# Kernel optimization log

Hardware: AMD Instinct MI355X
Metric: run time of the kernel (lower is better)

## Reference

```python
import jax, jax.numpy as jnp
import numpy as np

B, LQ, C = 4, 4096, 384
NH, NL, NP = 6, 1, 4
HL, WL = 64, 64
LV = HL * WL
DH = C // NH
EPS = 1e-6


def layer_norm(x, g, b):
    mu = jnp.mean(x, axis=-1, keepdims=True)
    var = jnp.mean(jnp.square(x - mu), axis=-1, keepdims=True)
    return (x - mu) * jax.lax.rsqrt(var + EPS) * g + b


def ms_deform_attn_core(value, spatial_shapes, level_start_index, loc, attn_w):
    # value [B,LV,NH,DH]; loc [B,LQ,NH,NL,NP,2] in [0,1]; attn_w [B,LQ,NH,NL,NP]
    ss = np.asarray(spatial_shapes)
    lsi = np.asarray(level_start_index)
    Bv, _, nH, dh = value.shape
    Lq = loc.shape[1]
    nP = loc.shape[4]
    out = jnp.zeros((Bv, Lq, nH, dh), value.dtype)
    for l in range(loc.shape[3]):
        Hl, Wl = int(ss[l, 0]), int(ss[l, 1])
        st = int(lsi[l])
        vflat = value[:, st:st + Hl * Wl]  # [B, Hl*Wl, nH, dh]
        xy = loc[:, :, :, l]               # [B,LQ,nH,NP,2]
        # grid_sample(align_corners=False): pixel = loc * size - 0.5
        x = xy[..., 0] * Wl - 0.5
        y = xy[..., 1] * Hl - 0.5
        x0 = jnp.floor(x)
        y0 = jnp.floor(y)
        wx = x - x0
        wy = y - y0
        x0i = x0.astype(jnp.int32)
        y0i = y0.astype(jnp.int32)

        def gather(xi, yi):
            # zero padding outside the feature map (padding_mode='zeros')
            valid = (xi >= 0) & (xi < Wl) & (yi >= 0) & (yi < Hl)
            idx = jnp.clip(yi, 0, Hl - 1) * Wl + jnp.clip(xi, 0, Wl - 1)  # [B,LQ,nH,NP]
            idx2 = idx.transpose(0, 1, 3, 2).reshape(Bv, Lq * nP, nH)
            g = jnp.take_along_axis(vflat, idx2[..., None], axis=1)       # [B,LQ*NP,nH,dh]
            g = g.reshape(Bv, Lq, nP, nH, dh).transpose(0, 1, 3, 2, 4)    # [B,LQ,nH,NP,dh]
            return g * valid[..., None].astype(value.dtype)

        samp = (gather(x0i, y0i) * ((1 - wx) * (1 - wy))[..., None]
                + gather(x0i + 1, y0i) * (wx * (1 - wy))[..., None]
                + gather(x0i, y0i + 1) * ((1 - wx) * wy)[..., None]
                + gather(x0i + 1, y0i + 1) * (wx * wy)[..., None])
        out = out + jnp.einsum('bqhpd,bqhp->bqhd', samp, attn_w[:, :, :, l])
    return out.reshape(Bv, Lq, nH * dh)


def setup_inputs() -> dict:
    key = jax.random.key(0)
    ks = jax.random.split(key, 12)
    s = 0.02
    return {
        'query': jax.random.normal(ks[0], (B, LQ, C), jnp.float32),
        'reference_points': jax.random.uniform(ks[1], (B, LQ, NL, 2), dtype=jnp.float32),
        'feat': jax.random.normal(ks[2], (B, LV, C), jnp.float32),
        'spatial_shapes': jnp.array([[HL, WL]], jnp.int32),
        'level_start_index': jnp.array([0], jnp.int32),
        'ln_q_g': jnp.ones((C,), jnp.float32), 'ln_q_b': jnp.zeros((C,), jnp.float32),
        'ln_f_g': jnp.ones((C,), jnp.float32), 'ln_f_b': jnp.zeros((C,), jnp.float32),
        'gamma': jax.random.normal(ks[3], (C,), jnp.float32) * 0.1,
        'Wv': jax.random.normal(ks[4], (C, C), jnp.float32) * s,
        'bv': jnp.zeros((C,), jnp.float32),
        'Wo': jax.random.normal(ks[5], (C, NH * NL * NP * 2), jnp.float32) * s,
        'bo': jax.random.normal(ks[6], (NH * NL * NP * 2,), jnp.float32) * 0.5,
        'Wa': jax.random.normal(ks[7], (C, NH * NL * NP), jnp.float32) * s,
        'ba': jnp.zeros((NH * NL * NP,), jnp.float32),
        'Wout': jax.random.normal(ks[8], (C, C), jnp.float32) * s,
        'bout': jnp.zeros((C,), jnp.float32),
    }


def reference(query, reference_points, feat, spatial_shapes, level_start_index,
              ln_q_g, ln_q_b, ln_f_g, ln_f_b, gamma,
              Wv, bv, Wo, bo, Wa, ba, Wout, bout):
    q = layer_norm(query, ln_q_g, ln_q_b)
    f = layer_norm(feat, ln_f_g, ln_f_b)
    value = (f @ Wv + bv).reshape(B, LV, NH, DH)
    offsets = (q @ Wo + bo).reshape(B, LQ, NH, NL, NP, 2)
    attn_w = jax.nn.softmax((q @ Wa + ba).reshape(B, LQ, NH, NL * NP), axis=-1)
    attn_w = attn_w.reshape(B, LQ, NH, NL, NP)
    # offset normalizer is (W, H) per level
    norm = jnp.stack([spatial_shapes[:, 1], spatial_shapes[:, 0]], -1).astype(jnp.float32)
    loc = reference_points[:, :, None, :, None, :] + offsets / norm[None, None, None, :, None, :]
    attn = ms_deform_attn_core(value, spatial_shapes, level_start_index, loc, attn_w)
    attn = attn @ Wout + bout
    return query + gamma * attn
```

## Files before the change

kernel.cpp:

```cpp
#include <hip/hip_runtime.h>
#include <math.h>

#define B_    4
#define LQ_   4096
#define C_    384
#define NH_   6
#define NP_   4
#define HL_   64
#define WL_   64
#define LV_   (HL_ * WL_)
#define ROWS_ (B_ * LQ_)
#define EPS_  1e-6f
#define NOFF_ 48
#define NLOG_ 24

typedef unsigned short u16;
typedef __bf16 bf16x8 __attribute__((ext_vector_type(8)));
typedef float  f32x4  __attribute__((ext_vector_type(4)));

__device__ __forceinline__ float bf2f(u16 v) {
    unsigned int u = ((unsigned int)v) << 16;
    return __uint_as_float(u);
}
__device__ __forceinline__ u16 f2bf(float f) {
    unsigned int u = __float_as_uint(f);
    u += 0x7fff + ((u >> 16) & 1);
    return (u16)(u >> 16);
}

__device__ __forceinline__ f32x4 mfma16(bf16x8 a, bf16x8 b, f32x4 c) {
    return __builtin_amdgcn_mfma_f32_16x16x32_bf16(a, b, c, 0, 0, 0);
}

__device__ __forceinline__ void gl_lds16(const u16* g, u16* l) {
    __builtin_amdgcn_global_load_lds(
        (const __attribute__((address_space(1))) unsigned int*)g,
        (__attribute__((address_space(3))) unsigned int*)l, 16, 0, 0);
}

#define LN_BLOCKS_   8192
#define PREP_BLOCKS_ 1273

__global__ __launch_bounds__(256) void ln_prep(
    const float* __restrict__ query, const float* __restrict__ feat,
    const float* __restrict__ qg, const float* __restrict__ qbv,
    const float* __restrict__ fg, const float* __restrict__ fbv,
    u16* __restrict__ qout, u16* __restrict__ fout,
    const float* __restrict__ Wv, const float* __restrict__ Wout,
    const float* __restrict__ Wo, const float* __restrict__ Wa,
    const float* __restrict__ bo, const float* __restrict__ ba,
    u16* __restrict__ WvT, u16* __restrict__ WoutT, u16* __restrict__ WcT,
    float* __restrict__ bias_c)
{
    if (blockIdx.x < LN_BLOCKS_) {
        int wid  = threadIdx.x >> 6;
        int lane = threadIdx.x & 63;
        int row  = blockIdx.x * 4 + wid;
        const float *src, *g, *bsh;
        u16* dst;
        int r;
        if (row < ROWS_) { src = query; g = qg; bsh = qbv; dst = qout; r = row; }
        else             { src = feat;  g = fg; bsh = fbv; dst = fout; r = row - ROWS_; }

        const float* x = src + (size_t)r * C_;
        float v[6];
        float s = 0.f;
#pragma unroll
        for (int k = 0; k < 6; ++k) { v[k] = x[lane + 64 * k]; s += v[k]; }
#pragma unroll
        for (int off = 32; off; off >>= 1) s += __shfl_xor(s, off);
        float mu = s * (1.f / C_);

        float s2 = 0.f;
#pragma unroll
        for (int k = 0; k < 6; ++k) { float d = v[k] - mu; s2 += d * d; }
#pragma unroll
        for (int off = 32; off; off >>= 1) s2 += __shfl_xor(s2, off);
        float rs = rsqrtf(s2 * (1.f / C_) + EPS_);

        u16* y = dst + (size_t)r * C_;
#pragma unroll
        for (int k = 0; k < 6; ++k) {
            int c = lane + 64 * k;
            y[c] = f2bf((v[k] - mu) * rs * g[c] + bsh[c]);
        }
    } else {
        const int KN = 384 * 384;
        int idx = (blockIdx.x - LN_BLOCKS_) * 256 + threadIdx.x;
        if (idx < KN) {
            int n = idx / 384, k = idx - n * 384;
            WvT[idx] = f2bf(Wv[k * 384 + n]);
        } else if (idx < 2 * KN) {
            int t = idx - KN;
            int n = t / 384, k = t - n * 384;
            WoutT[t] = f2bf(Wout[k * 384 + n]);
        } else if (idx < 2 * KN + 80 * 384) {
            int t = idx - 2 * KN;
            int n = t / 384, k = t - n * 384;
            float v = (n < 48) ? Wo[k * 48 + n] : (n < 72 ? Wa[k * 24 + (n - 48)] : 0.f);
            WcT[t] = f2bf(v);
        } else if (idx < 2 * KN + 80 * 384 + 80) {
            int n = idx - (2 * KN + 80 * 384);
            bias_c[n] = (n < 48) ? bo[n] : (n < 72 ? ba[n - 48] : 0.f);
        }
    }
}

__global__ __launch_bounds__(256) void gemm_combined(
    const u16* __restrict__ fb, const u16* __restrict__ qb,
    const u16* __restrict__ WvT, const u16* __restrict__ WcT,
    const float* __restrict__ bv, const float* __restrict__ bias_c,
    u16* __restrict__ valb, float* __restrict__ offs, float* __restrict__ logits)
{
    const int K = 384;
    __shared__ __align__(16) u16 As[128 * 32];
    __shared__ __align__(16) u16 Bs[128 * 32];

    int g    = blockIdx.x;
    int tid  = threadIdx.x;
    int lane = tid & 63, wid = tid >> 6;
    int fr = lane & 15, quad = lane >> 4;

    int srow = tid >> 2;
    int scol = (tid & 3) * 8;

    if (g < 384) {
        int m0 = (g / 3) * 128, n0 = (g % 3) * 128;
        const u16* agp0 = fb  + (size_t)(m0 + srow) * K + scol;
        const u16* agp1 = fb  + (size_t)(m0 + 64 + srow) * K + scol;
        const u16* bgp0 = WvT + (size_t)(n0 + srow) * K + scol;
        const u16* bgp1 = WvT + (size_t)(n0 + 64 + srow) * K + scol;
        u16* al0 = As + tid * 8;  u16* al1 = As + 2048 + tid * 8;
        u16* bl0 = Bs + tid * 8;  u16* bl1 = Bs + 2048 + tid * 8;

        int wm = (wid >> 1) * 64, wn = (wid & 1) * 64;

        f32x4 zero = {0.f, 0.f, 0.f, 0.f};
        f32x4 acc[4][4];
#pragma unroll
        for (int i = 0; i < 4; ++i)
#pragma unroll
            for (int j = 0; j < 4; ++j) acc[i][j] = zero;

        for (int k0 = 0; k0 < K; k0 += 32) {
            gl_lds16(agp0 + k0, al0);
            gl_lds16(agp1 + k0, al1);
            gl_lds16(bgp0 + k0, bl0);
            gl_lds16(bgp1 + k0, bl1);
            __syncthreads();
            bf16x8 af[4], bfr[4];
#pragma unroll
            for (int i = 0; i < 4; ++i)
                af[i] = *(bf16x8*)&As[(wm + i * 16 + fr) * 32 + quad * 8];
#pragma unroll
            for (int j = 0; j < 4; ++j)
                bfr[j] = *(bf16x8*)&Bs[(wn + j * 16 + fr) * 32 + quad * 8];
#pragma unroll
            for (int i = 0; i < 4; ++i)
#pragma unroll
                for (int j = 0; j < 4; ++j)
                    acc[i][j] = mfma16(af[i], bfr[j], acc[i][j]);
            __syncthreads();
        }

#pragma unroll
        for (int i = 0; i < 4; ++i) {
            int row = m0 + wm + i * 16 + quad * 4;
#pragma unroll
            for (int j = 0; j < 4; ++j) {
                int col = n0 + wn + j * 16 + fr;
                float bcol = bv[col];
#pragma unroll
                for (int r = 0; r < 4; ++r)
                    valb[(size_t)(row + r) * C_ + col] = f2bf(acc[i][j][r] + bcol);
            }
        }
    } else {
        int m0 = (g - 384) * 128;
        const u16* agp0 = qb + (size_t)(m0 + srow) * K + scol;
        const u16* agp1 = qb + (size_t)(m0 + 64 + srow) * K + scol;
        u16* al0 = As + tid * 8;  u16* al1 = As + 2048 + tid * 8;
        const u16* bgp0 = WcT + (size_t)srow * K + scol;
        const u16* bgp1 = WcT + (size_t)(64 + srow) * K + scol;
        u16* bl0 = Bs + tid * 8;
        u16* bl1 = Bs + 2048 + tid * 8;

        int wm = wid * 32;

        f32x4 zero = {0.f, 0.f, 0.f, 0.f};
        f32x4 acc[2][5];
#pragma unroll
        for (int i = 0; i < 2; ++i)
#pragma unroll
            for (int j = 0; j < 5; ++j) acc[i][j] = zero;

        for (int k0 = 0; k0 < K; k0 += 32) {
            gl_lds16(agp0 + k0, al0);
            gl_lds16(agp1 + k0, al1);
            gl_lds16(bgp0 + k0, bl0);
            if (tid < 64) gl_lds16(bgp1 + k0, bl1);
            __syncthreads();
            bf16x8 af[2], bfr[5];
#pragma unroll
            for (int i = 0; i < 2; ++i)
                af[i] = *(bf16x8*)&As[(wm + i * 16 + fr) * 32 + quad * 8];
#pragma unroll
            for (int j = 0; j < 5; ++j)
                bfr[j] = *(bf16x8*)&Bs[(j * 16 + fr) * 32 + quad * 8];
#pragma unroll
            for (int i = 0; i < 2; ++i)
#pragma unroll
                for (int j = 0; j < 5; ++j)
                    acc[i][j] = mfma16(af[i], bfr[j], acc[i][j]);
            __syncthreads();
        }

#pragma unroll
        for (int i = 0; i < 2; ++i) {
            int row = m0 + wm + i * 16 + quad * 4;
#pragma unroll
            for (int j = 0; j < 5; ++j) {
                int col = j * 16 + fr;
                if (col < 72) {
                    float bcol = bias_c[col];
#pragma unroll
                    for (int r = 0; r < 4; ++r) {
                        float v = acc[i][j][r] + bcol;
                        if (col < 48) offs[(size_t)(row + r) * NOFF_ + col] = v;
                        else          logits[(size_t)(row + r) * NLOG_ + (col - 48)] = v;
                    }
                }
            }
        }
    }
}

#define QT_   16
#define APAD_ 392

__global__ __launch_bounds__(512) void fused_sample_out(
    const u16*  __restrict__ value,
    const float* __restrict__ rp,
    const float* __restrict__ offs,
    const float* __restrict__ logits,
    const u16*  __restrict__ WoutT,
    const float* __restrict__ bout,
    const float* __restrict__ gamma,
    const float* __restrict__ query,
    float* __restrict__ out)
{
    __shared__ __align__(16) u16 attn_s[QT_ * APAD_];

    int t = threadIdx.x;
    int g = blockIdx.x;
    int b     = (g & 7) >> 1;
    int local = ((g >> 3) << 1) | (g & 1);
    int m0 = b * LQ_ + local * QT_;

    const u16* vbatch = value + (size_t)b * LV_ * C_;

#pragma unroll
    for (int j = 0; j < 2; ++j) {
        int v = t + 512 * j;
        if (v < QT_ * 48) {
            int q = v / 48, dc = v - q * 48;
            int h = dc >> 3;
            int col0 = dc << 3;
            int r = m0 + q;

            float4 lg  = *(const float4*)(logits + (size_t)r * NLOG_ + h * 4);
            float2 rpv = *(const float2*)(rp + (size_t)r * 2);
            float4 of0 = *(const float4*)(offs + (size_t)r * NOFF_ + h * 8);
            float4 of1 = *(const float4*)(offs + (size_t)r * NOFF_ + h * 8 + 4);

            float mx = fmaxf(fmaxf(lg.x, lg.y), fmaxf(lg.z, lg.w));
            float e0 = __expf(lg.x - mx), e1 = __expf(lg.y - mx);
            float e2 = __expf(lg.z - mx), e3 = __expf(lg.w - mx);
            float rden = 1.f / (e0 + e1 + e2 + e3);
            float aws[4] = {e0 * rden, e1 * rden, e2 * rden, e3 * rden};
            float oxs[4] = {of0.x, of0.z, of1.x, of1.z};
            float oys[4] = {of0.y, of0.w, of1.y, of1.w};

            const u16* vbase = vbatch + col0;
            float acc[8] = {0.f, 0.f, 0.f, 0.f, 0.f, 0.f, 0.f, 0.f};
#pragma unroll
            for (int p = 0; p < NP_; ++p) {
                float x = rpv.x * (float)WL_ + oxs[p] - 0.5f;
                float y = rpv.y * (float)HL_ + oys[p] - 0.5f;
                float x0f = floorf(x), y0f = floorf(y);
                float wx = x - x0f, wy = y - y0f;
                int x0 = (int)x0f, y0 = (int)y0f;
#pragma unroll
                for (int c = 0; c < 4; ++c) {
                    int xi = x0 + (c & 1);
                    int yi = y0 + (c >> 1);
                    bool valid = (xi >= 0) && (xi < WL_) && (yi >= 0) && (yi < HL_);
                    int xc = xi < 0 ? 0 : (xi > WL_ - 1 ? WL_ - 1 : xi);
                    int yc = yi < 0 ? 0 : (yi > HL_ - 1 ? HL_ - 1 : yi);
                    float w = ((c & 1) ? wx : 1.f - wx) * ((c >> 1) ? wy : 1.f - wy) * aws[p];
                    w = valid ? w : 0.f;
                    bf16x8 vv = *(const bf16x8*)(vbase + (size_t)(yc * WL_ + xc) * C_);
#pragma unroll
                    for (int e = 0; e < 8; ++e) acc[e] += w * (float)vv[e];
                }
            }
            u16* dst = attn_s + q * APAD_ + col0;
#pragma unroll
            for (int e = 0; e < 8; ++e) dst[e] = f2bf(acc[e]);
        }
    }
    __syncthreads();

    int lane = t & 63, wid = t >> 6;
    int fr = lane & 15, quad = lane >> 4;
    int wn0 = wid * 48;

    f32x4 zero = {0.f, 0.f, 0.f, 0.f};
    f32x4 acc[3];
#pragma unroll
    for (int j = 0; j < 3; ++j) acc[j] = zero;

    for (int k0 = 0; k0 < 384; k0 += 32) {
        bf16x8 a0 = *(bf16x8*)&attn_s[fr * APAD_ + k0 + quad * 8];
#pragma unroll
        for (int nt = 0; nt < 3; ++nt) {
            bf16x8 bb = *(const bf16x8*)(WoutT + (size_t)(wn0 + nt * 16 + fr) * 384 + k0 + quad * 8);
            acc[nt] = mfma16(a0, bb, acc[nt]);
        }
    }

#pragma unroll
    for (int nt = 0; nt < 3; ++nt) {
        int col = wn0 + nt * 16 + fr;
        float gm = gamma[col], bc = bout[col];
#pragma unroll
        for (int rr = 0; rr < 4; ++rr) {
            size_t o = (size_t)(m0 + quad * 4 + rr) * C_ + col;
            out[o] = query[o] + gm * (acc[nt][rr] + bc);
        }
    }
}

extern "C" void kernel_launch(void* const* d_in, const int* in_sizes, int n_in,
                              void* d_out, int out_size, void* d_ws, size_t ws_size,
                              hipStream_t stream)
{
    const float* query  = (const float*)d_in[0];
    const float* rp     = (const float*)d_in[1];
    const float* feat   = (const float*)d_in[2];
    const float* gamma  = (const float*)d_in[9];
    const float* Wv     = (const float*)d_in[10];
    const float* bv     = (const float*)d_in[11];
    const float* Wo     = (const float*)d_in[12];
    const float* bo     = (const float*)d_in[13];
    const float* Wa     = (const float*)d_in[14];
    const float* ba     = (const float*)d_in[15];
    const float* Wout   = (const float*)d_in[16];
    const float* bout   = (const float*)d_in[17];
    float* out = (float*)d_out;

    u16* wsu    = (u16*)d_ws;
    u16* qb     = wsu;
    u16* fb     = qb    + (size_t)ROWS_ * C_;
    u16* valb   = fb    + (size_t)ROWS_ * C_;
    u16* WvT    = valb  + (size_t)ROWS_ * C_;
    u16* WoutT  = WvT   + 384 * 384;
    u16* WcT    = WoutT + 384 * 384;
    float* offs   = (float*)(WcT + 80 * 384);
    float* logits = offs + (size_t)ROWS_ * NOFF_;
    float* bias_c = logits + (size_t)ROWS_ * NLOG_;

    ln_prep<<<LN_BLOCKS_ + PREP_BLOCKS_, 256, 0, stream>>>(
        query, feat,
        (const float*)d_in[5], (const float*)d_in[6],
        (const float*)d_in[7], (const float*)d_in[8],
        qb, fb, Wv, Wout, Wo, Wa, bo, ba, WvT, WoutT, WcT, bias_c);

    gemm_combined<<<512, 256, 0, stream>>>(fb, qb, WvT, WcT, bv, bias_c,
                                           valb, offs, logits);

    fused_sample_out<<<ROWS_ / QT_, 512, 0, stream>>>(
        valb, rp, offs, logits, WoutT, bout, gamma, query, out);
}
```

Before: 186.3 us.

## Split fused sampler/out-projection into separate sampler and tiled output GEMM

```diff
diff --git a/kernel.cpp b/kernel.cpp
--- a/kernel.cpp
+++ b/kernel.cpp
@@ -15,17 +15,17 @@
 #define NLOG_ 24
 
 typedef unsigned short u16;
+typedef unsigned int   u32;
 typedef __bf16 bf16x8 __attribute__((ext_vector_type(8)));
 typedef float  f32x4  __attribute__((ext_vector_type(4)));
 
-__device__ __forceinline__ float bf2f(u16 v) {
-    unsigned int u = ((unsigned int)v) << 16;
-    return __uint_as_float(u);
-}
 __device__ __forceinline__ u16 f2bf(float f) {
-    unsigned int u = __float_as_uint(f);
+    u32 u = __float_as_uint(f);
     u += 0x7fff + ((u >> 16) & 1);
     return (u16)(u >> 16);
+}
+__device__ __forceinline__ u32 pack2bf(float a, float b) {
+    return (u32)f2bf(a) | ((u32)f2bf(b) << 16);
 }
 
 __device__ __forceinline__ f32x4 mfma16(bf16x8 a, bf16x8 b, f32x4 c) {
@@ -63,27 +63,38 @@
         else             { src = feat;  g = fg; bsh = fbv; dst = fout; r = row - ROWS_; }
 
         const float* x = src + (size_t)r * C_;
-        float v[6];
-        float s = 0.f;
-#pragma unroll
-        for (int k = 0; k < 6; ++k) { v[k] = x[lane + 64 * k]; s += v[k]; }
+        float4 a4 = *(const float4*)(x + 4 * lane);
+        float2 a2 = *(const float2*)(x + 256 + 2 * lane);
+        float v0 = a4.x, v1 = a4.y, v2 = a4.z, v3 = a4.w, v4 = a2.x, v5 = a2.y;
+
+        float s = v0 + v1 + v2 + v3 + v4 + v5;
 #pragma unroll
         for (int off = 32; off; off >>= 1) s += __shfl_xor(s, off);
         float mu = s * (1.f / C_);
 
-        float s2 = 0.f;
-#pragma unroll
-        for (int k = 0; k < 6; ++k) { float d = v[k] - mu; s2 += d * d; }
+        float d0 = v0 - mu, d1 = v1 - mu, d2 = v2 - mu;
+        float d3 = v3 - mu, d4 = v4 - mu, d5 = v5 - mu;
+        float s2 = d0*d0 + d1*d1 + d2*d2 + d3*d3 + d4*d4 + d5*d5;
 #pragma unroll
         for (int off = 32; off; off >>= 1) s2 += __shfl_xor(s2, off);
         float rs = rsqrtf(s2 * (1.f / C_) + EPS_);
 
+        float4 g4 = *(const float4*)(g + 4 * lane);
+        float4 b4 = *(const float4*)(bsh + 4 * lane);
+        float2 g2 = *(const float2*)(g + 256 + 2 * lane);
+        float2 b2 = *(const float2*)(bsh + 256 + 2 * lane);
+
+        float o0 = d0 * rs * g4.x + b4.x;
+        float o1 = d1 * rs * g4.y + b4.y;
+        float o2 = d2 * rs * g4.z + b4.z;
+        float o3 = d3 * rs * g4.w + b4.w;
+        float o4 = d4 * rs * g2.x + b2.x;
+        float o5 = d5 * rs * g2.y + b2.y;
+
         u16* y = dst + (size_t)r * C_;
-#pragma unroll
-        for (int k = 0; k < 6; ++k) {
-            int c = lane + 64 * k;
-            y[c] = f2bf((v[k] - mu) * rs * g[c] + bsh[c]);
-        }
+        uint2 w0; w0.x = pack2bf(o0, o1); w0.y = pack2bf(o2, o3);
+        *(uint2*)(y + 4 * lane) = w0;
+        *(u32*)(y + 256 + 2 * lane) = pack2bf(o4, o5);
     } else {
         const int KN = 384 * 384;
         int idx = (blockIdx.x - LN_BLOCKS_) * 256 + threadIdx.x;
@@ -235,108 +246,134 @@
     }
 }
 
-#define QT_   16
-#define APAD_ 392
-
-__global__ __launch_bounds__(512) void fused_sample_out(
+__global__ __launch_bounds__(384) void sampler(
     const u16*  __restrict__ value,
     const float* __restrict__ rp,
     const float* __restrict__ offs,
     const float* __restrict__ logits,
-    const u16*  __restrict__ WoutT,
-    const float* __restrict__ bout,
-    const float* __restrict__ gamma,
-    const float* __restrict__ query,
-    float* __restrict__ out)
+    u16* __restrict__ attn)
 {
-    __shared__ __align__(16) u16 attn_s[QT_ * APAD_];
-
     int t = threadIdx.x;
     int g = blockIdx.x;
     int b     = (g & 7) >> 1;
     int local = ((g >> 3) << 1) | (g & 1);
-    int m0 = b * LQ_ + local * QT_;
-
-    const u16* vbatch = value + (size_t)b * LV_ * C_;
-
-#pragma unroll
-    for (int j = 0; j < 2; ++j) {
-        int v = t + 512 * j;
-        if (v < QT_ * 48) {
-            int q = v / 48, dc = v - q * 48;
-            int h = dc >> 3;
-            int col0 = dc << 3;
-            int r = m0 + q;
-
-            float4 lg  = *(const float4*)(logits + (size_t)r * NLOG_ + h * 4);
-            float2 rpv = *(const float2*)(rp + (size_t)r * 2);
-            float4 of0 = *(const float4*)(offs + (size_t)r * NOFF_ + h * 8);
-            float4 of1 = *(const float4*)(offs + (size_t)r * NOFF_ + h * 8 + 4);
-
-            float mx = fmaxf(fmaxf(lg.x, lg.y), fmaxf(lg.z, lg.w));
-            float e0 = __expf(lg.x - mx), e1 = __expf(lg.y - mx);
-            float e2 = __expf(lg.z - mx), e3 = __expf(lg.w - mx);
-            float rden = 1.f / (e0 + e1 + e2 + e3);
-            float aws[4] = {e0 * rden, e1 * rden, e2 * rden, e3 * rden};
-            float oxs[4] = {of0.x, of0.z, of1.x, of1.z};
-            float oys[4] = {of0.y, of0.w, of1.y, of1.w};
-
-            const u16* vbase = vbatch + col0;
-            float acc[8] = {0.f, 0.f, 0.f, 0.f, 0.f, 0.f, 0.f, 0.f};
-#pragma unroll
-            for (int p = 0; p < NP_; ++p) {
-                float x = rpv.x * (float)WL_ + oxs[p] - 0.5f;
-                float y = rpv.y * (float)HL_ + oys[p] - 0.5f;
-                float x0f = floorf(x), y0f = floorf(y);
-                float wx = x - x0f, wy = y - y0f;
-                int x0 = (int)x0f, y0 = (int)y0f;
-#pragma unroll
-                for (int c = 0; c < 4; ++c) {
-                    int xi = x0 + (c & 1);
-                    int yi = y0 + (c >> 1);
-                    bool valid = (xi >= 0) && (xi < WL_) && (yi >= 0) && (yi < HL_);
-                    int xc = xi < 0 ? 0 : (xi > WL_ - 1 ? WL_ - 1 : xi);
-                    int yc = yi < 0 ? 0 : (yi > HL_ - 1 ? HL_ - 1 : yi);
-                    float w = ((c & 1) ? wx : 1.f - wx) * ((c >> 1) ? wy : 1.f - wy) * aws[p];
-                    w = valid ? w : 0.f;
-                    bf16x8 vv = *(const bf16x8*)(vbase + (size_t)(yc * WL_ + xc) * C_);
-#pragma unroll
-                    for (int e = 0; e < 8; ++e) acc[e] += w * (float)vv[e];
-                }
+    int q  = t / 48, dc = t - q * 48;
+    int h  = dc >> 3;
+    int col0 = dc << 3;
+    int r  = b * LQ_ + local * 8 + q;
+
+    float4 lg  = *(const float4*)(logits + (size_t)r * NLOG_ + h * 4);
+    float2 rpv = *(const float2*)(rp + (size_t)r * 2);
+    float4 of0 = *(const float4*)(offs + (size_t)r * NOFF_ + h * 8);
+    float4 of1 = *(const float4*)(offs + (size_t)r * NOFF_ + h * 8 + 4);
+
+    float mx = fmaxf(fmaxf(lg.x, lg.y), fmaxf(lg.z, lg.w));
+    float e0 = __expf(lg.x - mx), e1 = __expf(lg.y - mx);
+    float e2 = __expf(lg.z - mx), e3 = __expf(lg.w - mx);
+    float rden = 1.f / (e0 + e1 + e2 + e3);
+    float aws[4] = {e0 * rden, e1 * rden, e2 * rden, e3 * rden};
+    float oxs[4] = {of0.x, of0.z, of1.x, of1.z};
+    float oys[4] = {of0.y, of0.w, of1.y, of1.w};
+
+    const u16* vbase = value + (size_t)b * LV_ * C_ + col0;
+    float acc[8] = {0.f, 0.f, 0.f, 0.f, 0.f, 0.f, 0.f, 0.f};
+#pragma unroll
+    for (int p = 0; p < NP_; ++p) {
+        float x = rpv.x * (float)WL_ + oxs[p] - 0.5f;
+        float y = rpv.y * (float)HL_ + oys[p] - 0.5f;
+        float x0f = floorf(x), y0f = floorf(y);
+        float wx = x - x0f, wy = y - y0f;
+        int x0 = (int)x0f, y0 = (int)y0f;
+#pragma unroll
+        for (int c = 0; c < 4; ++c) {
+            int xi = x0 + (c & 1);
+            int yi = y0 + (c >> 1);
+            bool valid = (xi >= 0) && (xi < WL_) && (yi >= 0) && (yi < HL_);
+            int xc = xi < 0 ? 0 : (xi > WL_ - 1 ? WL_ - 1 : xi);
+            int yc = yi < 0 ? 0 : (yi > HL_ - 1 ? HL_ - 1 : yi);
+            float w = ((c & 1) ? wx : 1.f - wx) * ((c >> 1) ? wy : 1.f - wy) * aws[p];
+            w = valid ? w : 0.f;
+            bf16x8 vv = *(const bf16x8*)(vbase + (size_t)(yc * WL_ + xc) * C_);
+#pragma unroll
+            for (int e = 0; e < 8; ++e) acc[e] += w * (float)vv[e];
+        }
+    }
+
+    uint4 o;
+    o.x = pack2bf(acc[0], acc[1]);
+    o.y = pack2bf(acc[2], acc[3]);
+    o.z = pack2bf(acc[4], acc[5]);
+    o.w = pack2bf(acc[6], acc[7]);
+    *(uint4*)(attn + (size_t)r * C_ + col0) = o;
+}
+
+__global__ __launch_bounds__(256) void out_gemm(
+    const u16* __restrict__ A, const u16* __restrict__ Bt,
+    const float* __restrict__ bout, const float* __restrict__ gamma,
+    const float* __restrict__ query, float* __restrict__ out)
+{
+    const int K = 384;
+    __shared__ __align__(16) u16 As[128 * 32];
+    __shared__ __align__(16) u16 Bs[128 * 32];
+
+    int g    = blockIdx.x;
+    int tid  = threadIdx.x;
+    int lane = tid & 63, wid = tid >> 6;
+    int fr = lane & 15, quad = lane >> 4;
+
+    int srow = tid >> 2;
+    int scol = (tid & 3) * 8;
+
+    int m0 = (g / 3) * 128, n0 = (g % 3) * 128;
+    const u16* agp0 = A  + (size_t)(m0 + srow) * K + scol;
+    const u16* agp1 = A  + (size_t)(m0 + 64 + srow) * K + scol;
+    const u16* bgp0 = Bt + (size_t)(n0 + srow) * K + scol;
+    const u16* bgp1 = Bt + (size_t)(n0 + 64 + srow) * K + scol;
+    u16* al0 = As + tid * 8;  u16* al1 = As + 2048 + tid * 8;
+    u16* bl0 = Bs + tid * 8;  u16* bl1 = Bs + 2048 + tid * 8;
+
+    int wm = (wid >> 1) * 64, wn = (wid & 1) * 64;
+
+    f32x4 zero = {0.f, 0.f, 0.f, 0.f};
+    f32x4 acc[4][4];
+#pragma unroll
+    for (int i = 0; i < 4; ++i)
+#pragma unroll
+        for (int j = 0; j < 4; ++j) acc[i][j] = zero;
+
+    for (int k0 = 0; k0 < K; k0 += 32) {
+        gl_lds16(agp0 + k0, al0);
+        gl_lds16(agp1 + k0, al1);
+        gl_lds16(bgp0 + k0, bl0);
+        gl_lds16(bgp1 + k0, bl1);
+        __syncthreads();
+        bf16x8 af[4], bfr[4];
+#pragma unroll
+        for (int i = 0; i < 4; ++i)
+            af[i] = *(bf16x8*)&As[(wm + i * 16 + fr) * 32 + quad * 8];
+#pragma unroll
+        for (int j = 0; j < 4; ++j)
+            bfr[j] = *(bf16x8*)&Bs[(wn + j * 16 + fr) * 32 + quad * 8];
+#pragma unroll
+        for (int i = 0; i < 4; ++i)
+#pragma unroll
+            for (int j = 0; j < 4; ++j)
+                acc[i][j] = mfma16(af[i], bfr[j], acc[i][j]);
+        __syncthreads();
+    }
+
+#pragma unroll
+    for (int i = 0; i < 4; ++i) {
+        int row = m0 + wm + i * 16 + quad * 4;
+#pragma unroll
+        for (int j = 0; j < 4; ++j) {
+            int col = n0 + wn + j * 16 + fr;
+            float bc = bout[col], gm = gamma[col];
+#pragma unroll
+            for (int r = 0; r < 4; ++r) {
+                size_t o = (size_t)(row + r) * C_ + col;
+                out[o] = query[o] + gm * (acc[i][j][r] + bc);
             }
-            u16* dst = attn_s + q * APAD_ + col0;
-#pragma unroll
-            for (int e = 0; e < 8; ++e) dst[e] = f2bf(acc[e]);
-        }
-    }
-    __syncthreads();
-
-    int lane = t & 63, wid = t >> 6;
-    int fr = lane & 15, quad = lane >> 4;
-    int wn0 = wid * 48;
-
-    f32x4 zero = {0.f, 0.f, 0.f, 0.f};
-    f32x4 acc[3];
-#pragma unroll
-    for (int j = 0; j < 3; ++j) acc[j] = zero;
-
-    for (int k0 = 0; k0 < 384; k0 += 32) {
-        bf16x8 a0 = *(bf16x8*)&attn_s[fr * APAD_ + k0 + quad * 8];
-#pragma unroll
-        for (int nt = 0; nt < 3; ++nt) {
-            bf16x8 bb = *(const bf16x8*)(WoutT + (size_t)(wn0 + nt * 16 + fr) * 384 + k0 + quad * 8);
-            acc[nt] = mfma16(a0, bb, acc[nt]);
-        }
-    }
-
-#pragma unroll
-    for (int nt = 0; nt < 3; ++nt) {
-        int col = wn0 + nt * 16 + fr;
-        float gm = gamma[col], bc = bout[col];
-#pragma unroll
-        for (int rr = 0; rr < 4; ++rr) {
-            size_t o = (size_t)(m0 + quad * 4 + rr) * C_ + col;
-            out[o] = query[o] + gm * (acc[nt][rr] + bc);
         }
     }
 }
@@ -363,7 +400,8 @@
     u16* qb     = wsu;
     u16* fb     = qb    + (size_t)ROWS_ * C_;
     u16* valb   = fb    + (size_t)ROWS_ * C_;
-    u16* WvT    = valb  + (size_t)ROWS_ * C_;
+    u16* attnb  = valb  + (size_t)ROWS_ * C_;
+    u16* WvT    = attnb + (size_t)ROWS_ * C_;
     u16* WoutT  = WvT   + 384 * 384;
     u16* WcT    = WoutT + 384 * 384;
     float* offs   = (float*)(WcT + 80 * 384);
@@ -379,6 +417,7 @@
     gemm_combined<<<512, 256, 0, stream>>>(fb, qb, WvT, WcT, bv, bias_c,
                                            valb, offs, logits);
 
-    fused_sample_out<<<ROWS_ / QT_, 512, 0, stream>>>(
-        valb, rp, offs, logits, WoutT, bout, gamma, query, out);
-}
+    sampler<<<2048, 384, 0, stream>>>(valb, rp, offs, logits, attnb);
+
+    out_gemm<<<384, 256, 0, stream>>>(attnb, WoutT, bout, gamma, query, out);
+}
```

Result: faster. 173.3 us (-7.0%).
